# Kernel optimization log

Hardware: AMD Instinct MI355X
Metric: run time of the kernel (lower is better)

## Reference

```python
import jax, jax.numpy as jnp
import numpy as np

EPS = 1e-5


def _bn(x, gamma, beta, mean, var):
    # Inference-mode BatchNorm2d over channel dim (NCHW -> axis 1).
    inv = gamma / jnp.sqrt(var + EPS)
    return x * inv[None, :, None, None] + (beta - mean * inv)[None, :, None, None]


def setup_inputs() -> dict:
    key = jax.random.key(0)
    ks = jax.random.split(key, 6)
    N, Cin, Cout, T, V = 64, 64, 128, 300, 25
    x = jax.random.normal(ks[0], (N, Cin, T, V), dtype=jnp.float32)
    A = jax.random.uniform(ks[1], (V, V), dtype=jnp.float32)  # fixed adjacency (non-trainable buffer)
    edge = jnp.ones((V, V), dtype=jnp.float32)                # learnable edge mask, init ones
    gcn_w = jax.random.normal(ks[2], (Cout, Cin), dtype=jnp.float32) * 0.05
    gcn_b = jnp.zeros((Cout,), dtype=jnp.float32)
    res_w = jax.random.normal(ks[3], (Cout, Cin), dtype=jnp.float32) * 0.05
    res_b = jnp.zeros((Cout,), dtype=jnp.float32)
    return {
        'x': x, 'A': A, 'edge': edge,
        'gcn_w': gcn_w, 'gcn_b': gcn_b,
        'bn_gamma': jnp.ones((Cout,), jnp.float32), 'bn_beta': jnp.zeros((Cout,), jnp.float32),
        'bn_mean': jnp.zeros((Cout,), jnp.float32), 'bn_var': jnp.ones((Cout,), jnp.float32),
        'res_w': res_w, 'res_b': res_b,
        'rbn_gamma': jnp.ones((Cout,), jnp.float32), 'rbn_beta': jnp.zeros((Cout,), jnp.float32),
        'rbn_mean': jnp.zeros((Cout,), jnp.float32), 'rbn_var': jnp.ones((Cout,), jnp.float32),
    }


def reference(x, A, edge, gcn_w, gcn_b, bn_gamma, bn_beta, bn_mean, bn_var,
              res_w, res_b, rbn_gamma, rbn_beta, rbn_mean, rbn_var):
    # x: [N, Cin, T, V]
    # residual branch: 1x1 conv + BN (in_channel != out_channel path)
    res = jnp.einsum('oc,nctv->notv', res_w, x) + res_b[None, :, None, None]
    res = _bn(res, rbn_gamma, rbn_beta, rbn_mean, rbn_var)
    # main branch: 1x1 conv -> adjacency einsum -> BN
    y = jnp.einsum('oc,nctv->notv', gcn_w, x) + gcn_b[None, :, None, None]
    y = jnp.einsum('nctv,vw->nctw', y, A * edge)
    y = _bn(y, bn_gamma, bn_beta, bn_mean, bn_var)
    # keep_prob = 1.0 -> Randomized_DropBlock_Ske / DropBlockT_1d are identity
    return jax.nn.relu(y + res)
```

## Files before the change

### kernel.cpp

```cpp
#include <hip/hip_runtime.h>
#include <stdint.h>

#define N_ 64
#define C_ 64
#define O_ 128
#define T_ 300
#define V_ 25
#define TB 4
#define JB (TB * 32)
#define KB 128
#define LDB 136
#define SXS 65
#define BS_OFF 26000
#define SMEM_BYTES (BS_OFF + JB * LDB * 2)
#define STW 3200

typedef __attribute__((ext_vector_type(8))) short short8;
typedef __attribute__((ext_vector_type(4))) float floatx4;

__device__ __forceinline__ short f2bf(float f) {
  unsigned u = __float_as_uint(f);
  unsigned r = (u + 0x7FFFu + ((u >> 16) & 1u)) >> 16;
  return (short)(r & 0xFFFFu);
}

__global__ void sgc_prep(const float* __restrict__ A, const float* __restrict__ edge,
                         const float* __restrict__ gcn_w, const float* __restrict__ gcn_b,
                         const float* __restrict__ bn_g, const float* __restrict__ bn_b,
                         const float* __restrict__ bn_m, const float* __restrict__ bn_v,
                         const float* __restrict__ res_w, const float* __restrict__ res_b,
                         const float* __restrict__ rg, const float* __restrict__ rb,
                         const float* __restrict__ rm, const float* __restrict__ rv,
                         short* __restrict__ Wcat, float* __restrict__ M2p,
                         float* __restrict__ Cwp) {
  const int tid = threadIdx.x;
  for (int i = tid; i < 25 * 32; i += 256) {
    const int v = i >> 5, w = i & 31;
    M2p[i] = (w < 25) ? A[v * 25 + w] * edge[v * 25 + w] : 0.f;
  }
  for (int i = tid; i < O_ * 32; i += 256) {
    const int o = i >> 5, w = i & 31;
    const float inv1 = bn_g[o] * rsqrtf(bn_v[o] + 1e-5f);
    const float inv2 = rg[o] * rsqrtf(rv[o] + 1e-5f);
    float S = 0.f;
    if (w < 25) {
      for (int v = 0; v < 25; ++v) S += A[v * 25 + w] * edge[v * 25 + w];
    }
    Cwp[i] = inv1 * gcn_b[o] * S + (bn_b[o] - bn_m[o] * inv1) + inv2 * res_b[o] +
             (rb[o] - rm[o] * inv2);
  }
  for (int i = tid; i < O_ * KB; i += 256) {
    const int o = i >> 7, k = i & 127;
    const float inv1 = bn_g[o] * rsqrtf(bn_v[o] + 1e-5f);
    const float inv2 = rg[o] * rsqrtf(rv[o] + 1e-5f);
    const float val = (k < 64) ? inv2 * res_w[o * 64 + k] : inv1 * gcn_w[o * 64 + (k - 64)];
    Wcat[i] = f2bf(val);
  }
}

__global__ __launch_bounds__(256, 2) void sgc_main(const float* __restrict__ x,
                                                   const short* __restrict__ Wcat,
                                                   const float* __restrict__ M2p,
                                                   const float* __restrict__ Cw,
                                                   float* __restrict__ out) {
  __shared__ __align__(16) char smem[SMEM_BYTES];
  float* const xs = (float*)smem;
  short* const Bs = (short*)(smem + BS_OFF);

  const int tid = threadIdx.x;
  const int b = blockIdx.x;
  const int n = b / 75;
  const int t0 = (b % 75) * TB;
  const int lane = tid & 63;
  const int wv = tid >> 6;
  const int l15 = lane & 15;
  const int quad = lane >> 4;
  const int obase = wv * 32;

  short8 af[2][4];
#pragma unroll
  for (int mt = 0; mt < 2; ++mt) {
#pragma unroll
    for (int kq = 0; kq < 4; ++kq) {
      af[mt][kq] =
          *(const short8*)(Wcat + (obase + mt * 16 + l15) * KB + kq * 32 + quad * 8);
    }
  }

  {
    const float* xbase = x + n * (C_ * T_ * V_) + t0 * V_;
    for (int u = tid; u < 1600; u += 256) {
      const int c = u / 25;
      const int q = u - c * 25;
      const floatx4 vv = *(const floatx4*)(xbase + c * (T_ * V_) + q * 4);
      const int a0 = (q * 4) * SXS + c;
#pragma unroll
      for (int i = 0; i < 4; ++i) xs[a0 + i * SXS] = vv[i];
    }
    for (int u = tid; u < 448; u += 256) {
      const int row = u >> 4;
      const int col = u & 15;
      const int tl = row / 7;
      const int v = 25 + (row - tl * 7);
      *(floatx4*)(Bs + (tl * 32 + v) * LDB + col * 8) = (floatx4){0.f, 0.f, 0.f, 0.f};
    }
  }
  __syncthreads();

  {
    const int tl = wv;
    const int c = lane;
    float xr[25];
#pragma unroll
    for (int v = 0; v < 25; ++v) xr[v] = xs[(tl * 25 + v) * SXS + c];
#pragma unroll
    for (int v = 0; v < 25; ++v) Bs[(tl * 32 + v) * LDB + c] = f2bf(xr[v]);
    float xa[25];
#pragma unroll
    for (int w = 0; w < 25; ++w) xa[w] = 0.f;
    for (int v = 0; v < 25; ++v) {
      const float xv = xr[v];
      const float* m2 = M2p + v * 32;
#pragma unroll
      for (int w = 0; w < 25; ++w) xa[w] = __builtin_fmaf(xv, m2[w], xa[w]);
    }
#pragma unroll
    for (int w = 0; w < 25; ++w) Bs[(tl * 32 + w) * LDB + 64 + c] = f2bf(xa[w]);
  }
  __syncthreads();

  floatx4 acc[2][8];
#pragma unroll
  for (int mt = 0; mt < 2; ++mt)
#pragma unroll
    for (int jt = 0; jt < 8; ++jt) acc[mt][jt] = (floatx4){0.f, 0.f, 0.f, 0.f};

#pragma unroll
  for (int jt = 0; jt < 8; ++jt) {
#pragma unroll
    for (int kq = 0; kq < 4; ++kq) {
      const short8 bf =
          *(const short8*)(&Bs[(jt * 16 + l15) * LDB + kq * 32 + quad * 8]);
      acc[0][jt] = __builtin_amdgcn_mfma_f32_16x16x32_bf16(af[0][kq], bf, acc[0][jt], 0, 0, 0);
      acc[1][jt] = __builtin_amdgcn_mfma_f32_16x16x32_bf16(af[1][kq], bf, acc[1][jt], 0, 0, 0);
    }
  }
  __syncthreads();

  {
    float* const st = (float*)smem + wv * STW;
#pragma unroll
    for (int mt = 0; mt < 2; ++mt) {
#pragma unroll
      for (int jt = 0; jt < 8; ++jt) {
        const int j = jt * 16 + l15;
        const int w = j & 31;
        if (w < 25) {
          const int tloc = j >> 5;
          const int ol0 = mt * 16 + quad * 4;
          const float* cwp = Cw + (obase + ol0) * 32 + w;
          float* sp = st + ol0 * 100 + tloc * 25 + w;
#pragma unroll
          for (int r = 0; r < 4; ++r) {
            const float val = acc[mt][jt][r] + cwp[r * 32];
            sp[r * 100] = val > 0.f ? val : 0.f;
          }
        }
      }
    }
  }
  __syncthreads();

  {
    float* const st = (float*)smem + wv * STW;
    float* const ob = out + ((n * O_ + obase) * T_ + t0) * V_;
    for (int u = lane; u < 800; u += 64) {
      const int ol = u / 25;
      const int q = u - ol * 25;
      *(floatx4*)(ob + ol * (T_ * V_) + q * 4) = *(const floatx4*)(st + ol * 100 + q * 4);
    }
  }
}

extern "C" void kernel_launch(void* const* d_in, const int* in_sizes, int n_in,
                              void* d_out, int out_size, void* d_ws, size_t ws_size,
                              hipStream_t stream) {
  const float* x = (const float*)d_in[0];
  const float* A = (const float*)d_in[1];
  const float* edge = (const float*)d_in[2];
  const float* gcn_w = (const float*)d_in[3];
  const float* gcn_b = (const float*)d_in[4];
  const float* bn_g = (const float*)d_in[5];
  const float* bn_b = (const float*)d_in[6];
  const float* bn_m = (const float*)d_in[7];
  const float* bn_v = (const float*)d_in[8];
  const float* res_w = (const float*)d_in[9];
  const float* res_b = (const float*)d_in[10];
  const float* rg = (const float*)d_in[11];
  const float* rb = (const float*)d_in[12];
  const float* rm = (const float*)d_in[13];
  const float* rv = (const float*)d_in[14];

  char* ws = (char*)d_ws;
  short* Wcat = (short*)(ws);
  float* M2p = (float*)(ws + 32768);
  float* Cwp = (float*)(ws + 36864);
  float* out = (float*)d_out;

  hipLaunchKernelGGL(sgc_prep, dim3(1), dim3(256), 0, stream, A, edge, gcn_w, gcn_b,
                     bn_g, bn_b, bn_m, bn_v, res_w, res_b, rg, rb, rm, rv, Wcat, M2p, Cwp);
  hipLaunchKernelGGL(sgc_main, dim3(N_ * (T_ / TB)), dim3(256), 0, stream, x, Wcat, M2p,
                     Cwp, out);
}
```

Before: 528.1 us.

## Halve time tile per block, raise occupancy, split adjacency work across waves

Each block now covers 2 time steps instead of 4. That doubles the grid and shrinks shared memory, and the launch bounds now ask for 4 blocks per CU. The adjacency multiply is split so that pairs of waves each compute about half of the 25 output joints. The explicit zeroing of the padding rows is dropped. The last block barrier becomes a wave-local LDS wait, since each wave reads back only its own staging region. The aim is more parallelism to hide latency in this memory-bound kernel, at the cost of narrower 8-byte global loads and stores and more per-block overhead.

```diff
diff --git a/kernel.cpp b/kernel.cpp
--- a/kernel.cpp
+++ b/kernel.cpp
@@ -6,17 +6,18 @@
 #define O_ 128
 #define T_ 300
 #define V_ 25
-#define TB 4
+#define TB 2
 #define JB (TB * 32)
 #define KB 128
 #define LDB 136
 #define SXS 65
-#define BS_OFF 26000
+#define BS_OFF 13056
 #define SMEM_BYTES (BS_OFF + JB * LDB * 2)
-#define STW 3200
+#define STW 1600
 
 typedef __attribute__((ext_vector_type(8))) short short8;
 typedef __attribute__((ext_vector_type(4))) float floatx4;
+typedef __attribute__((ext_vector_type(2))) float floatx2;
 
 __device__ __forceinline__ short f2bf(float f) {
   unsigned u = __float_as_uint(f);
@@ -58,7 +59,7 @@
   }
 }
 
-__global__ __launch_bounds__(256, 2) void sgc_main(const float* __restrict__ x,
+__global__ __launch_bounds__(256, 4) void sgc_main(const float* __restrict__ x,
                                                    const short* __restrict__ Wcat,
                                                    const float* __restrict__ M2p,
                                                    const float* __restrict__ Cw,
@@ -69,8 +70,8 @@
 
   const int tid = threadIdx.x;
   const int b = blockIdx.x;
-  const int n = b / 75;
-  const int t0 = (b % 75) * TB;
+  const int n = b / 150;
+  const int t0 = (b % 150) * TB;
   const int lane = tid & 63;
   const int wv = tid >> 6;
   const int l15 = lane & 15;
@@ -92,51 +93,46 @@
     for (int u = tid; u < 1600; u += 256) {
       const int c = u / 25;
       const int q = u - c * 25;
-      const floatx4 vv = *(const floatx4*)(xbase + c * (T_ * V_) + q * 4);
-      const int a0 = (q * 4) * SXS + c;
-#pragma unroll
-      for (int i = 0; i < 4; ++i) xs[a0 + i * SXS] = vv[i];
-    }
-    for (int u = tid; u < 448; u += 256) {
-      const int row = u >> 4;
-      const int col = u & 15;
-      const int tl = row / 7;
-      const int v = 25 + (row - tl * 7);
-      *(floatx4*)(Bs + (tl * 32 + v) * LDB + col * 8) = (floatx4){0.f, 0.f, 0.f, 0.f};
+      const floatx2 vv = *(const floatx2*)(xbase + c * (T_ * V_) + q * 2);
+      const int a0 = (q * 2) * SXS + c;
+      xs[a0] = vv[0];
+      xs[a0 + SXS] = vv[1];
     }
   }
   __syncthreads();
 
   {
-    const int tl = wv;
-    const int c = lane;
+    const int c = tid & 63;
+    const int tl = (tid >> 6) & 1;
+    const int h = tid >> 7;
+    const int w0 = h * 12;
     float xr[25];
 #pragma unroll
     for (int v = 0; v < 25; ++v) xr[v] = xs[(tl * 25 + v) * SXS + c];
 #pragma unroll
-    for (int v = 0; v < 25; ++v) Bs[(tl * 32 + v) * LDB + c] = f2bf(xr[v]);
-    float xa[25];
-#pragma unroll
-    for (int w = 0; w < 25; ++w) xa[w] = 0.f;
+    for (int i = 0; i < 13; ++i) Bs[(tl * 32 + w0 + i) * LDB + c] = f2bf(xr[w0 + i]);
+    float xa[13];
+#pragma unroll
+    for (int i = 0; i < 13; ++i) xa[i] = 0.f;
     for (int v = 0; v < 25; ++v) {
       const float xv = xr[v];
-      const float* m2 = M2p + v * 32;
-#pragma unroll
-      for (int w = 0; w < 25; ++w) xa[w] = __builtin_fmaf(xv, m2[w], xa[w]);
-    }
-#pragma unroll
-    for (int w = 0; w < 25; ++w) Bs[(tl * 32 + w) * LDB + 64 + c] = f2bf(xa[w]);
+      const float* m2 = M2p + v * 32 + w0;
+#pragma unroll
+      for (int i = 0; i < 13; ++i) xa[i] = __builtin_fmaf(xv, m2[i], xa[i]);
+    }
+#pragma unroll
+    for (int i = 0; i < 13; ++i) Bs[(tl * 32 + w0 + i) * LDB + 64 + c] = f2bf(xa[i]);
   }
   __syncthreads();
 
-  floatx4 acc[2][8];
+  floatx4 acc[2][4];
 #pragma unroll
   for (int mt = 0; mt < 2; ++mt)
 #pragma unroll
-    for (int jt = 0; jt < 8; ++jt) acc[mt][jt] = (floatx4){0.f, 0.f, 0.f, 0.f};
-
-#pragma unroll
-  for (int jt = 0; jt < 8; ++jt) {
+    for (int jt = 0; jt < 4; ++jt) acc[mt][jt] = (floatx4){0.f, 0.f, 0.f, 0.f};
+
+#pragma unroll
+  for (int jt = 0; jt < 4; ++jt) {
 #pragma unroll
     for (int kq = 0; kq < 4; ++kq) {
       const short8 bf =
@@ -152,24 +148,24 @@
 #pragma unroll
     for (int mt = 0; mt < 2; ++mt) {
 #pragma unroll
-      for (int jt = 0; jt < 8; ++jt) {
+      for (int jt = 0; jt < 4; ++jt) {
         const int j = jt * 16 + l15;
         const int w = j & 31;
         if (w < 25) {
           const int tloc = j >> 5;
           const int ol0 = mt * 16 + quad * 4;
           const float* cwp = Cw + (obase + ol0) * 32 + w;
-          float* sp = st + ol0 * 100 + tloc * 25 + w;
+          float* sp = st + ol0 * 50 + tloc * 25 + w;
 #pragma unroll
           for (int r = 0; r < 4; ++r) {
             const float val = acc[mt][jt][r] + cwp[r * 32];
-            sp[r * 100] = val > 0.f ? val : 0.f;
+            sp[r * 50] = val > 0.f ? val : 0.f;
           }
         }
       }
     }
   }
-  __syncthreads();
+  asm volatile("s_waitcnt lgkmcnt(0)" ::: "memory");
 
   {
     float* const st = (float*)smem + wv * STW;
@@ -177,7 +173,7 @@
     for (int u = lane; u < 800; u += 64) {
       const int ol = u / 25;
       const int q = u - ol * 25;
-      *(floatx4*)(ob + ol * (T_ * V_) + q * 4) = *(const floatx4*)(st + ol * 100 + q * 4);
+      *(floatx2*)(ob + ol * (T_ * V_) + q * 2) = *(const floatx2*)(st + ol * 50 + q * 2);
     }
   }
 }
```

Measured after the change: 603.1 us. 14.2% more time.
